# Kernel optimization log

Hardware: AMD Instinct MI355X
Metric: run time of the kernel (lower is better)

The kernel has to match this reference:

```python
import jax, jax.numpy as jnp
import numpy as np

SIGMA = 10
POPULATIONS = 2
LR = 0.001


def _normalize(L, prior):
    # clamp then normalize over populations (logsumexp across the population axis)
    O = L.shape[1]
    L = jnp.clip(L, -5.0, 0.0)
    lse = jax.nn.logsumexp(L.reshape(POPULATIONS, -1, O), axis=0)  # (in/P, O)
    L = L - jnp.tile(lse, (POPULATIONS, 1))
    prior = jnp.clip(prior, -5.0, 0.0)
    prior = prior - jax.nn.logsumexp(prior)
    return L, prior


def _forward(x, L, prior):
    B, T, IN = x.shape
    O = L.shape[1]
    L, prior = _normalize(L, prior)  # matches normalize_probs() in __init__

    # membrane potential: OR of spikes over trailing window of SIGMA steps
    xb = x.astype(bool)
    pot = xb
    for s in range(1, SIGMA):  # fixed small loop (sigma=10)
        pot = pot | jnp.pad(xb, ((0, 0), (s, 0), (0, 0)))[:, :T, :]

    tpre0 = jnp.full((B, IN), -T, dtype=jnp.int32)
    tpost0 = jnp.full((B, O), jnp.iinfo(jnp.int32).max, dtype=jnp.int32)
    base_key = jax.random.key(42)

    pot_T = jnp.transpose(pot, (1, 0, 2))  # (T,B,IN)
    x_T = jnp.transpose(xb, (1, 0, 2))

    def step(carry, inp):
        L, prior, tpre, tpost, t = carry
        pot_t, x_t = inp
        potf = pot_t.astype(L.dtype)
        logits = potf @ L + prior  # (B,O), logits <= 0 so exp is safe
        # torch: softmax(exp(logits)).multinomial == categorical with logits=exp(logits)
        key = jax.random.fold_in(base_key, t)
        widx = jax.random.categorical(key, jnp.exp(logits), axis=-1)  # (B,)
        win = jax.nn.one_hot(widx, O, dtype=L.dtype)
        # trace updates happen BEFORE STDP, as in the torch code
        tpre = jnp.where(x_t, 0, tpre - 1)
        tpost = jnp.where(win > 0, 0, tpost - 1)
        ltp = (tpre >= -SIGMA).astype(L.dtype)
        ltd = (tpre < -SIGMA).astype(L.dtype)
        post = (tpost < 0).astype(L.dtype)
        m_ltp = jnp.einsum('bi,bo->io', ltp, win) / B
        m_ltd = jnp.einsum('bi,bo->io', ltd, win) / B
        m_pp = jnp.einsum('bi,bo->io', potf, post) / B
        decay = (t + 1).astype(L.dtype)  # lr_decay_inverse starts at 1
        # dw = (5 e^{-L} - 1) * LTP.mean - LTD.mean - pre_post.mean ; LTD was negated
        dw = (5.0 * jnp.exp(-L) - 1.0) * m_ltp + m_ltd - m_pp
        L2 = L + (LR / decay) * dw
        wm = jnp.mean(win, axis=0)
        db = (-5.0 * prior - 1.0) * wm - (1.0 - wm)
        p2 = prior + (LR / decay) * db
        L2, p2 = _normalize(L2, p2)
        return (L2, p2, tpre, tpost, t + 1), None

    (Lf, pf, _, _, _), _ = jax.lax.scan(
        step, (L, prior, tpre0, tpost0, jnp.int32(0)), (pot_T, x_T))
    return jnp.concatenate([Lf.reshape(-1), pf])


def setup_inputs() -> dict:
    key = jax.random.key(0)
    k1, k2, k3 = jax.random.split(key, 3)
    B, T, IN, O = 256, 200, 1568, 100
    x = jax.random.randint(k1, (B, T, IN), 0, 2, dtype=jnp.int32)
    log_likelihood = jax.random.uniform(k2, (IN, O), dtype=jnp.float32) * -1.0 - 1.0
    log_prior = jax.random.uniform(k3, (O,), dtype=jnp.float32) * -1.0 - 1.0
    return {"x": x, "log_likelihood": log_likelihood, "log_prior": log_prior}


def reference(x, log_likelihood, log_prior):
    return _forward(x, log_likelihood, log_prior)
```

## Files before the change

kernel.cpp:

```cpp
#include <hip/hip_runtime.h>
#include <stdint.h>

#define BB 256
#define TT 200
#define INN 1568
#define OO 100
#define PAIRS 784
#define NHALF 12800

typedef unsigned long long u64;

__device__ __forceinline__ void tf_round(uint32_t& x0, uint32_t& x1, int r) {
    x0 += x1;
    x1 = (x1 << r) | (x1 >> (32 - r));
    x1 ^= x0;
}

__device__ __forceinline__ void threefry(uint32_t k0, uint32_t k1,
                                         uint32_t x0, uint32_t x1,
                                         uint32_t& o0, uint32_t& o1) {
    uint32_t k2 = k0 ^ k1 ^ 0x1BD11BDAu;
    x0 += k0; x1 += k1;
    tf_round(x0,x1,13); tf_round(x0,x1,15); tf_round(x0,x1,26); tf_round(x0,x1,6);
    x0 += k1; x1 += k2 + 1u;
    tf_round(x0,x1,17); tf_round(x0,x1,29); tf_round(x0,x1,16); tf_round(x0,x1,24);
    x0 += k2; x1 += k0 + 2u;
    tf_round(x0,x1,13); tf_round(x0,x1,15); tf_round(x0,x1,26); tf_round(x0,x1,6);
    x0 += k0; x1 += k1 + 3u;
    tf_round(x0,x1,17); tf_round(x0,x1,29); tf_round(x0,x1,16); tf_round(x0,x1,24);
    x0 += k1; x1 += k2 + 4u;
    tf_round(x0,x1,13); tf_round(x0,x1,15); tf_round(x0,x1,26); tf_round(x0,x1,6);
    o0 = x0 + k2; o1 = x1 + k0 + 5u;
}

__global__ __launch_bounds__(256) void k_winbit(const int* __restrict__ x,
                                                uint8_t* __restrict__ widx,
                                                u64* __restrict__ bitB) {
    if (blockIdx.x < 200) {
        int idx = blockIdx.x * 256 + threadIdx.x;
        int t = idx >> 8, b = idx & 255;
        uint32_t fk0, fk1;
        threefry(0u, 42u, 0u, (uint32_t)t, fk0, fk1);
        float best = -1e38f;
        int bo = 0;
        int nbase = b * OO;
        for (int o = 0; o < OO; ++o) {
            uint32_t n = (uint32_t)(nbase + o);
            uint32_t lo = (n < NHALF) ? n : n - NHALF;
            uint32_t v0, v1;
            threefry(fk0, fk1, lo, lo + NHALF, v0, v1);
            uint32_t bits = (n < NHALF) ? v0 : v1;
            uint32_t fb = (bits >> 9) | 0x3F800000u;
            float f = __uint_as_float(fb) - 1.0f;
            float u = (f == 0.0f) ? 1.17549435e-38f : f;
            float g = -logf(-logf(u));
            if (g > best) { best = g; bo = o; }
        }
        widx[idx] = (uint8_t)bo;
    } else {
        int idx = (blockIdx.x - 200) * 256 + threadIdx.x;
        if (idx >= 4 * TT * 392) return;
        int wb = idx / (TT * 392);
        int r = idx - wb * (TT * 392);
        int t = r / 392;
        int ig = r - t * 392;
        const int4* xp = (const int4*)x;
        u64 m0 = 0, m1 = 0, m2 = 0, m3 = 0;
        for (int j = 0; j < 64; ++j) {
            int b = wb * 64 + j;
            int4 v = xp[((size_t)b * TT + t) * 392 + ig];
            u64 bit = 1ull << j;
            if (v.x) m0 |= bit;
            if (v.y) m1 |= bit;
            if (v.z) m2 |= bit;
            if (v.w) m3 |= bit;
        }
        u64* dst = bitB + ((size_t)(t * 4 + wb)) * INN + 4 * ig;
        dst[0] = m0; dst[1] = m1; dst[2] = m2; dst[3] = m3;
    }
}

__global__ __launch_bounds__(256) void k_fwpost(const uint8_t* __restrict__ widx,
                                                u64* __restrict__ winbits,
                                                u64* __restrict__ postbits,
                                                uint32_t* __restrict__ cnt) {
    __shared__ uint32_t wl32[TT * 65];
    __shared__ int fwl[BB];
    int o = blockIdx.x;
    int tid = threadIdx.x;
    const uint32_t* wsrc = (const uint32_t*)widx;
    for (int g = tid; g < TT * 64; g += 256) {
        int t = g >> 6, w = g & 63;
        wl32[t * 65 + w] = wsrc[g];
    }
    __syncthreads();
    if (tid < 64) {
        int f0 = 255, f1 = 255, f2 = 255, f3 = 255;
        for (int t = 0; t < TT; ++t) {
            uint32_t w4 = wl32[t * 65 + tid];
            if (((w4      ) & 255u) == (uint32_t)o && f0 == 255) f0 = t;
            if (((w4 >>  8) & 255u) == (uint32_t)o && f1 == 255) f1 = t;
            if (((w4 >> 16) & 255u) == (uint32_t)o && f2 == 255) f2 = t;
            if (((w4 >> 24) & 255u) == (uint32_t)o && f3 == 255) f3 = t;
        }
        fwl[4 * tid + 0] = f0; fwl[4 * tid + 1] = f1;
        fwl[4 * tid + 2] = f2; fwl[4 * tid + 3] = f3;
    }
    __syncthreads();
    if (tid < TT) {
        int t = tid;
        u64 wbA[4], pbA[4];
        uint32_t c = 0;
        #pragma unroll
        for (int k = 0; k < 4; ++k) {
            u64 wacc = 0, pacc = 0;
            for (int q2 = 0; q2 < 16; ++q2) {
                uint32_t w4 = wl32[t * 65 + k * 16 + q2];
                #pragma unroll
                for (int j = 0; j < 4; ++j) {
                    int bl = q2 * 4 + j;
                    bool win = (((w4 >> (8 * j)) & 255u) == (uint32_t)o);
                    c += win ? 1u : 0u;
                    bool post = (fwl[k * 64 + q2 * 4 + j] < t) && !win;
                    u64 bit = 1ull << bl;
                    if (win)  wacc |= bit;
                    if (post) pacc |= bit;
                }
            }
            wbA[k] = wacc; pbA[k] = pacc;
        }
        size_t base = (size_t)(t * OO + o) * 4;
        #pragma unroll
        for (int k = 0; k < 4; ++k) {
            winbits[base + k] = wbA[k];
            postbits[base + k] = pbA[k];
        }
        cnt[t * OO + o] = c;
    }
}

__global__ __launch_bounds__(256) void k_popcW(
        const u64* __restrict__ bitB,
        const u64* __restrict__ winbits,
        const u64* __restrict__ postbits,
        uint2* __restrict__ packed,
        int t0) {
    __shared__ u64 winS[OO * 4];
    __shared__ u64 postS[OO * 4];
    int tl = blockIdx.y;
    int t = t0 + tl;
    int tid = threadIdx.x;
    for (int idx = tid; idx < OO * 4; idx += 256) {
        winS[idx]  = winbits[(size_t)t * OO * 4 + idx];
        postS[idx] = postbits[(size_t)t * OO * 4 + idx];
    }
    __syncthreads();
    int p = blockIdx.x * 256 + tid;
    if (p >= PAIRS) return;
    int i0 = p, i1 = p + PAIRS;
    u64 p0=0,p1=0,p2=0,p3=0,p4=0,p5=0,p6=0,p7=0;
    int ttlo = (t - 9 < 0) ? 0 : t - 9;
    for (int tt = ttlo; tt <= t; ++tt) {
        const u64* row = bitB + (size_t)tt * 4 * INN;
        p0 |= row[i0];           p1 |= row[INN + i0];
        p2 |= row[2 * INN + i0]; p3 |= row[3 * INN + i0];
        p4 |= row[i1];           p5 |= row[INN + i1];
        p6 |= row[2 * INN + i1]; p7 |= row[3 * INN + i1];
    }
    u64 l0=p0,l1=p1,l2=p2,l3=p3,l4=p4,l5=p5,l6=p6,l7=p7;
    if (t >= 10) {
        const u64* row = bitB + (size_t)(t - 10) * 4 * INN;
        l0 |= row[i0];           l1 |= row[INN + i0];
        l2 |= row[2 * INN + i0]; l3 |= row[3 * INN + i0];
        l4 |= row[i1];           l5 |= row[INN + i1];
        l6 |= row[2 * INN + i1]; l7 |= row[3 * INN + i1];
    }
    uint2* orow = packed + (size_t)tl * OO * PAIRS + p;
    #pragma unroll 4
    for (int o = 0; o < OO; ++o) {
        const u64* w = &winS[o * 4];
        const u64* s = &postS[o * 4];
        uint32_t lt0 = __popcll(l0 & w[0]) + __popcll(l1 & w[1])
                     + __popcll(l2 & w[2]) + __popcll(l3 & w[3]);
        uint32_t lt1 = __popcll(l4 & w[0]) + __popcll(l5 & w[1])
                     + __popcll(l6 & w[2]) + __popcll(l7 & w[3]);
        uint32_t pp0 = __popcll(p0 & s[0]) + __popcll(p1 & s[1])
                     + __popcll(p2 & s[2]) + __popcll(p3 & s[3]);
        uint32_t pp1 = __popcll(p4 & s[0]) + __popcll(p5 & s[1])
                     + __popcll(p6 & s[2]) + __popcll(p7 & s[3]);
        orow[(size_t)o * PAIRS] = make_uint2(lt0 | (pp0 << 16), lt1 | (pp1 << 16));
    }
}

__global__ __launch_bounds__(256) void k_chainsPrior(
        const float* __restrict__ L0,
        const float* __restrict__ p0arr,
        const uint2* __restrict__ packed,
        const uint32_t* __restrict__ cnt,
        float* __restrict__ outL,
        float* __restrict__ outp,
        int t0, int ct, int first, int do_prior) {
    if (blockIdx.y == OO) {
        if (!do_prior || blockIdx.x != 0 || threadIdx.x >= 64) return;
        int l = threadIdx.x;
        bool has2 = (l + 64) < OO;
        float pa = p0arr[l];
        float pb = has2 ? p0arr[l + 64] : -1e30f;
        auto normalize = [&]() {
            pa = fminf(fmaxf(pa, -5.0f), 0.0f);
            if (has2) pb = fminf(fmaxf(pb, -5.0f), 0.0f);
            float mx = has2 ? fmaxf(pa, pb) : pa;
            #pragma unroll
            for (int s = 32; s > 0; s >>= 1) mx = fmaxf(mx, __shfl_xor(mx, s, 64));
            float sm = expf(pa - mx) + (has2 ? expf(pb - mx) : 0.0f);
            #pragma unroll
            for (int s = 32; s > 0; s >>= 1) sm += __shfl_xor(sm, s, 64);
            float lse = logf(sm) + mx;
            pa -= lse;
            if (has2) pb -= lse;
        };
        normalize();
        for (int t = 0; t < TT; ++t) {
            float eta = 0.001f / (float)(t + 1);
            float wma = (float)cnt[t * OO + l] * (1.0f / 256.0f);
            pa += eta * ((-5.0f * pa - 1.0f) * wma - (1.0f - wma));
            if (has2) {
                float wmb = (float)cnt[t * OO + l + 64] * (1.0f / 256.0f);
                pb += eta * ((-5.0f * pb - 1.0f) * wmb - (1.0f - wmb));
            }
            normalize();
        }
        outp[l] = pa;
        if (has2) outp[l + 64] = pb;
        return;
    }
    int o = blockIdx.y;
    int p = blockIdx.x * blockDim.x + threadIdx.x;
    if (p >= PAIRS) return;
    int i0 = p, i1 = p + PAIRS;
    float a, b2;
    if (first) {
        a  = L0[(size_t)i0 * OO + o];
        b2 = L0[(size_t)i1 * OO + o];
        a  = fminf(fmaxf(a,  -5.0f), 0.0f);
        b2 = fminf(fmaxf(b2, -5.0f), 0.0f);
        float m = fmaxf(a, b2), mn = fminf(a, b2);
        float lse = __logf(1.0f + __expf(mn - m)) + m;
        a -= lse; b2 -= lse;
    } else {
        a  = outL[(size_t)i0 * OO + o];
        b2 = outL[(size_t)i1 * OO + o];
    }
    const uint2* src = packed + (size_t)o * PAIRS + p;
    const size_t tstride = (size_t)OO * PAIRS;
    uint2 c[6];
    #pragma unroll
    for (int k = 0; k < 6; ++k) {
        int idx = (k < ct) ? k : (ct - 1);
        c[k] = src[(size_t)idx * tstride];
    }
    #pragma unroll 6
    for (int tl = 0; tl < ct; ++tl) {
        uint2 cur = c[tl % 6];
        int nx = tl + 6; if (nx >= ct) nx = ct - 1;
        c[tl % 6] = src[(size_t)nx * tstride];
        int t = t0 + tl;
        float cwin = (float)cnt[t * OO + o];
        float lt0 = (float)(cur.x & 0xFFFFu), pp0 = (float)(cur.x >> 16);
        float lt1 = (float)(cur.y & 0xFFFFu), pp1 = (float)(cur.y >> 16);
        float eta = 0.001f / (float)(t + 1);
        float dw0 = (5.0f * __expf(-a)  - 1.0f) * (lt0 * (1.0f/256.0f))
                  + (cwin - lt0 - pp0) * (1.0f/256.0f);
        float dw1 = (5.0f * __expf(-b2) - 1.0f) * (lt1 * (1.0f/256.0f))
                  + (cwin - lt1 - pp1) * (1.0f/256.0f);
        a  += eta * dw0;
        b2 += eta * dw1;
        a  = fminf(fmaxf(a,  -5.0f), 0.0f);
        b2 = fminf(fmaxf(b2, -5.0f), 0.0f);
        float m = fmaxf(a, b2), mn = fminf(a, b2);
        float lse = __logf(1.0f + __expf(mn - m)) + m;
        a -= lse; b2 -= lse;
    }
    outL[(size_t)i0 * OO + o] = a;
    outL[(size_t)i1 * OO + o] = b2;
}

extern "C" void kernel_launch(void* const* d_in, const int* in_sizes, int n_in,
                              void* d_out, int out_size, void* d_ws, size_t ws_size,
                              hipStream_t stream) {
    const int*   x  = (const int*)d_in[0];
    const float* L0 = (const float*)d_in[1];
    const float* p0 = (const float*)d_in[2];
    float* out = (float*)d_out;

    char* ws = (char*)d_ws;
    size_t off = 0;
    auto alloc = [&](size_t bytes) -> void* {
        off = (off + 255) & ~(size_t)255;
        void* p = ws + off;
        off += bytes;
        return p;
    };
    uint8_t*  widx     = (uint8_t*) alloc((size_t)TT * BB);
    uint32_t* cnt      = (uint32_t*)alloc((size_t)TT * OO * 4);
    u64*      winbits  = (u64*)     alloc((size_t)TT * OO * 4 * 8);
    u64*      postbits = (u64*)     alloc((size_t)TT * OO * 4 * 8);
    u64*      bitB     = (u64*)     alloc((size_t)TT * 4 * INN * 8);

    static const int cands[] = {200, 100, 50, 25, 20, 10, 8, 5, 4, 2, 1};
    int CT = 1;
    size_t base_off = (off + 255) & ~(size_t)255;
    for (int c = 0; c < 11; ++c) {
        size_t need = base_off + (size_t)cands[c] * OO * PAIRS * sizeof(uint2);
        if (need <= ws_size) { CT = cands[c]; break; }
    }
    uint2* packed = (uint2*)(ws + base_off);

    hipLaunchKernelGGL(k_winbit, dim3(200 + (4 * TT * 392 + 255) / 256), dim3(256),
                       0, stream, x, widx, bitB);
    hipLaunchKernelGGL(k_fwpost, dim3(OO), dim3(256), 0, stream,
                       widx, winbits, postbits, cnt);
    for (int t0 = 0; t0 < TT; t0 += CT) {
        int ct = (t0 + CT <= TT) ? CT : (TT - t0);
        int last = (t0 + ct >= TT) ? 1 : 0;
        hipLaunchKernelGGL(k_popcW, dim3((PAIRS + 255) / 256, ct), dim3(256), 0, stream,
                           bitB, winbits, postbits, packed, t0);
        hipLaunchKernelGGL(k_chainsPrior, dim3((PAIRS + 255) / 256, OO + 1), dim3(256),
                           0, stream, L0, p0, packed, cnt, out,
                           out + (size_t)INN * OO, t0, ct, (t0 == 0) ? 1 : 0, last);
    }
}
```

Measured before the change: 662.9 us.

## Pack popcount counts into bytes and shrink blocks to 64 threads

```diff
diff --git a/kernel.cpp b/kernel.cpp
--- a/kernel.cpp
+++ b/kernel.cpp
@@ -33,11 +33,11 @@
     o0 = x0 + k2; o1 = x1 + k0 + 5u;
 }
 
-__global__ __launch_bounds__(256) void k_winbit(const int* __restrict__ x,
-                                                uint8_t* __restrict__ widx,
-                                                u64* __restrict__ bitB) {
-    if (blockIdx.x < 200) {
-        int idx = blockIdx.x * 256 + threadIdx.x;
+__global__ __launch_bounds__(64) void k_winbit(const int* __restrict__ x,
+                                               uint8_t* __restrict__ widx,
+                                               u64* __restrict__ bitB) {
+    if (blockIdx.x < 800) {
+        int idx = blockIdx.x * 64 + threadIdx.x;
         int t = idx >> 8, b = idx & 255;
         uint32_t fk0, fk1;
         threefry(0u, 42u, 0u, (uint32_t)t, fk0, fk1);
@@ -58,8 +58,7 @@
         }
         widx[idx] = (uint8_t)bo;
     } else {
-        int idx = (blockIdx.x - 200) * 256 + threadIdx.x;
-        if (idx >= 4 * TT * 392) return;
+        int idx = (blockIdx.x - 800) * 64 + threadIdx.x;
         int wb = idx / (TT * 392);
         int r = idx - wb * (TT * 392);
         int t = r / 392;
@@ -139,23 +138,23 @@
     }
 }
 
-__global__ __launch_bounds__(256) void k_popcW(
+__global__ __launch_bounds__(64) void k_popcW(
         const u64* __restrict__ bitB,
         const u64* __restrict__ winbits,
         const u64* __restrict__ postbits,
-        uint2* __restrict__ packed,
+        uint32_t* __restrict__ packed,
         int t0) {
     __shared__ u64 winS[OO * 4];
     __shared__ u64 postS[OO * 4];
     int tl = blockIdx.y;
     int t = t0 + tl;
     int tid = threadIdx.x;
-    for (int idx = tid; idx < OO * 4; idx += 256) {
+    for (int idx = tid; idx < OO * 4; idx += 64) {
         winS[idx]  = winbits[(size_t)t * OO * 4 + idx];
         postS[idx] = postbits[(size_t)t * OO * 4 + idx];
     }
     __syncthreads();
-    int p = blockIdx.x * 256 + tid;
+    int p = blockIdx.x * 64 + tid;
     if (p >= PAIRS) return;
     int i0 = p, i1 = p + PAIRS;
     u64 p0=0,p1=0,p2=0,p3=0,p4=0,p5=0,p6=0,p7=0;
@@ -175,7 +174,7 @@
         l4 |= row[i1];           l5 |= row[INN + i1];
         l6 |= row[2 * INN + i1]; l7 |= row[3 * INN + i1];
     }
-    uint2* orow = packed + (size_t)tl * OO * PAIRS + p;
+    uint32_t* orow = packed + (size_t)tl * OO * PAIRS + p;
     #pragma unroll 4
     for (int o = 0; o < OO; ++o) {
         const u64* w = &winS[o * 4];
@@ -188,20 +187,23 @@
                      + __popcll(p2 & s[2]) + __popcll(p3 & s[3]);
         uint32_t pp1 = __popcll(p4 & s[0]) + __popcll(p5 & s[1])
                      + __popcll(p6 & s[2]) + __popcll(p7 & s[3]);
-        orow[(size_t)o * PAIRS] = make_uint2(lt0 | (pp0 << 16), lt1 | (pp1 << 16));
-    }
-}
-
-__global__ __launch_bounds__(256) void k_chainsPrior(
+        lt0 = (lt0 > 255u) ? 255u : lt0;  pp0 = (pp0 > 255u) ? 255u : pp0;
+        lt1 = (lt1 > 255u) ? 255u : lt1;  pp1 = (pp1 > 255u) ? 255u : pp1;
+        uint32_t v = lt0 | (pp0 << 8) | (lt1 << 16) | (pp1 << 24);
+        __builtin_nontemporal_store(v, &orow[(size_t)o * PAIRS]);
+    }
+}
+
+__global__ __launch_bounds__(64) void k_chainsPrior(
         const float* __restrict__ L0,
         const float* __restrict__ p0arr,
-        const uint2* __restrict__ packed,
+        const uint32_t* __restrict__ packed,
         const uint32_t* __restrict__ cnt,
         float* __restrict__ outL,
         float* __restrict__ outp,
         int t0, int ct, int first, int do_prior) {
     if (blockIdx.y == OO) {
-        if (!do_prior || blockIdx.x != 0 || threadIdx.x >= 64) return;
+        if (!do_prior || blockIdx.x != 0) return;
         int l = threadIdx.x;
         bool has2 = (l + 64) < OO;
         float pa = p0arr[l];
@@ -235,7 +237,7 @@
         return;
     }
     int o = blockIdx.y;
-    int p = blockIdx.x * blockDim.x + threadIdx.x;
+    int p = blockIdx.x * 64 + threadIdx.x;
     if (p >= PAIRS) return;
     int i0 = p, i1 = p + PAIRS;
     float a, b2;
@@ -251,23 +253,23 @@
         a  = outL[(size_t)i0 * OO + o];
         b2 = outL[(size_t)i1 * OO + o];
     }
-    const uint2* src = packed + (size_t)o * PAIRS + p;
+    const uint32_t* src = packed + (size_t)o * PAIRS + p;
     const size_t tstride = (size_t)OO * PAIRS;
-    uint2 c[6];
+    uint32_t c[8];
     #pragma unroll
-    for (int k = 0; k < 6; ++k) {
+    for (int k = 0; k < 8; ++k) {
         int idx = (k < ct) ? k : (ct - 1);
-        c[k] = src[(size_t)idx * tstride];
-    }
-    #pragma unroll 6
+        c[k] = __builtin_nontemporal_load(&src[(size_t)idx * tstride]);
+    }
+    #pragma unroll 8
     for (int tl = 0; tl < ct; ++tl) {
-        uint2 cur = c[tl % 6];
-        int nx = tl + 6; if (nx >= ct) nx = ct - 1;
-        c[tl % 6] = src[(size_t)nx * tstride];
+        uint32_t cur = c[tl & 7];
+        int nx = tl + 8; if (nx >= ct) nx = ct - 1;
+        c[tl & 7] = __builtin_nontemporal_load(&src[(size_t)nx * tstride]);
         int t = t0 + tl;
         float cwin = (float)cnt[t * OO + o];
-        float lt0 = (float)(cur.x & 0xFFFFu), pp0 = (float)(cur.x >> 16);
-        float lt1 = (float)(cur.y & 0xFFFFu), pp1 = (float)(cur.y >> 16);
+        float lt0 = (float)(cur & 255u),         pp0 = (float)((cur >> 8) & 255u);
+        float lt1 = (float)((cur >> 16) & 255u), pp1 = (float)(cur >> 24);
         float eta = 0.001f / (float)(t + 1);
         float dw0 = (5.0f * __expf(-a)  - 1.0f) * (lt0 * (1.0f/256.0f))
                   + (cwin - lt0 - pp0) * (1.0f/256.0f);
@@ -311,21 +313,20 @@
     int CT = 1;
     size_t base_off = (off + 255) & ~(size_t)255;
     for (int c = 0; c < 11; ++c) {
-        size_t need = base_off + (size_t)cands[c] * OO * PAIRS * sizeof(uint2);
+        size_t need = base_off + (size_t)cands[c] * OO * PAIRS * 4;
         if (need <= ws_size) { CT = cands[c]; break; }
     }
-    uint2* packed = (uint2*)(ws + base_off);
-
-    hipLaunchKernelGGL(k_winbit, dim3(200 + (4 * TT * 392 + 255) / 256), dim3(256),
-                       0, stream, x, widx, bitB);
+    uint32_t* packed = (uint32_t*)(ws + base_off);
+
+    hipLaunchKernelGGL(k_winbit, dim3(800 + 4900), dim3(64), 0, stream, x, widx, bitB);
     hipLaunchKernelGGL(k_fwpost, dim3(OO), dim3(256), 0, stream,
                        widx, winbits, postbits, cnt);
     for (int t0 = 0; t0 < TT; t0 += CT) {
         int ct = (t0 + CT <= TT) ? CT : (TT - t0);
         int last = (t0 + ct >= TT) ? 1 : 0;
-        hipLaunchKernelGGL(k_popcW, dim3((PAIRS + 255) / 256, ct), dim3(256), 0, stream,
+        hipLaunchKernelGGL(k_popcW, dim3((PAIRS + 63) / 64, ct), dim3(64), 0, stream,
                            bitB, winbits, postbits, packed, t0);
-        hipLaunchKernelGGL(k_chainsPrior, dim3((PAIRS + 255) / 256, OO + 1), dim3(256),
+        hipLaunchKernelGGL(k_chainsPrior, dim3((PAIRS + 63) / 64, OO + 1), dim3(64),
                            0, stream, L0, p0, packed, cnt, out,
                            out + (size_t)INN * OO, t0, ct, (t0 == 0) ? 1 : 0, last);
     }
```

Measured after the change: 656.6 us. Within noise of the previous version (-1.0%).
